# Performance work log

Measured on AMD Instinct MI355X. Metric: run time of the kernel, lower is better.

## Reference

```python
import jax, jax.numpy as jnp
import numpy as np

HIDDEN = 1024
NUM_HEADS = 16
HEAD_SIZE = HIDDEN // NUM_HEADS


def setup_inputs() -> dict:
    key = jax.random.key(0)
    k1, k2, k3 = jax.random.split(key, 3)
    B, S = 2, 2048
    x = jax.random.normal(k1, (B, S, HIDDEN), dtype=jnp.float32)
    # query projection (source reuses it for both q and k)
    Wq = jax.random.normal(k2, (HIDDEN, HIDDEN), dtype=jnp.float32) / np.sqrt(HIDDEN)
    bq = jax.random.normal(k3, (HIDDEN,), dtype=jnp.float32) * 0.01
    return {"x": x, "Wq": Wq, "bq": bq}


def reference(x, Wq, bq):
    B, S, _ = x.shape
    # NOTE: source bug-for-bug: k uses the query projection too
    q = x @ Wq + bq                      # [B,S,D]
    k = x @ Wq + bq                      # [B,S,D]
    q = q.reshape(B, S, NUM_HEADS, HEAD_SIZE)
    k = k.reshape(B, S, NUM_HEADS, HEAD_SIZE)
    # scores: [B,H,S,S]
    e = jnp.einsum("bqhd,bkhd->bhqk", q, k)
    s = jax.nn.softmax(e / jnp.sqrt(jnp.float32(HEAD_SIZE)), axis=-1)
    return s
```

## Files before the change

### kernel.cpp

```cpp
#include <hip/hip_runtime.h>

#define HIDDEN 1024
#define SEQ 2048
#define NB 2
#define PSTRIDE 2052
#define NT 16

typedef _Float16 half8 __attribute__((ext_vector_type(8)));
typedef _Float16 half4 __attribute__((ext_vector_type(4)));
typedef float f32x4 __attribute__((ext_vector_type(4)));

#define GL2LDS(gp, lp) __builtin_amdgcn_global_load_lds( \
    (const __attribute__((address_space(1))) void*)(gp), \
    (__attribute__((address_space(3))) void*)(lp), 16, 0, 0)

__global__ __launch_bounds__(256) void cast_wt(const float* __restrict__ w,
                                               _Float16* __restrict__ wt) {
    __shared__ float tile[32][33];
    int bx = blockIdx.x * 32, by = blockIdx.y * 32;
    int tx = threadIdx.x, ty = threadIdx.y;
    #pragma unroll
    for (int i = 0; i < 32; i += 8)
        tile[ty + i][tx] = w[(by + ty + i) * HIDDEN + bx + tx];
    __syncthreads();
    #pragma unroll
    for (int i = 0; i < 32; i += 8)
        wt[(bx + ty + i) * HIDDEN + by + tx] = (_Float16)tile[tx][ty + i];
}

__global__ __launch_bounds__(512) void proj_gemm(const float* __restrict__ X,
                                                 const _Float16* __restrict__ Bt,
                                                 const float* __restrict__ bias,
                                                 _Float16* __restrict__ Q) {
    __shared__ _Float16 As[128 * 64];
    __shared__ _Float16 Bs[128 * 64];
    const int m0 = blockIdx.x * 128;
    const int n0 = blockIdx.y * 128;
    const int tid = threadIdx.x;
    const int w = tid >> 6, l = tid & 63;
    const int wm = w >> 2, wn = w & 3;
    const int lrow = l & 15, lkslot = l >> 4;

    const int srow = l >> 3, sslot = l & 7;

    f32x4 acc[4][2] = {};

    for (int k0 = 0; k0 < HIDDEN; k0 += 64) {
        __syncthreads();
        #pragma unroll
        for (int j = 0; j < 2; ++j) {
            const int chunk = w * 2 + j;
            const int r = chunk * 8 + srow;
            const int gslot = sslot ^ (r & 7);
            GL2LDS(&Bt[(size_t)(n0 + r) * HIDDEN + k0 + gslot * 8], Bs + chunk * 512);
        }
        #pragma unroll
        for (int it = 0; it < 2; ++it) {
            const int id = it * 512 + tid;
            const int row = id >> 3, slot = id & 7;
            const float* src = &X[(size_t)(m0 + row) * HIDDEN + k0 + slot * 8];
            f32x4 v0 = *(const f32x4*)src;
            f32x4 v1 = *(const f32x4*)(src + 4);
            half8 hv;
            hv[0] = (_Float16)v0[0]; hv[1] = (_Float16)v0[1];
            hv[2] = (_Float16)v0[2]; hv[3] = (_Float16)v0[3];
            hv[4] = (_Float16)v1[0]; hv[5] = (_Float16)v1[1];
            hv[6] = (_Float16)v1[2]; hv[7] = (_Float16)v1[3];
            *(half8*)&As[row * 64 + (slot ^ (row & 7)) * 8] = hv;
        }
        __syncthreads();
        #pragma unroll
        for (int kk = 0; kk < 64; kk += 32) {
            const int csb = kk >> 3;
            half8 af[4], bf[2];
            #pragma unroll
            for (int m = 0; m < 4; ++m) {
                const int R = wm * 64 + m * 16 + lrow;
                const int slot = (csb + lkslot) ^ (R & 7);
                af[m] = *(const half8*)&As[R * 64 + slot * 8];
            }
            #pragma unroll
            for (int n = 0; n < 2; ++n) {
                const int R = wn * 32 + n * 16 + lrow;
                const int slot = (csb + lkslot) ^ (R & 7);
                bf[n] = *(const half8*)&Bs[R * 64 + slot * 8];
            }
            #pragma unroll
            for (int m = 0; m < 4; ++m)
                #pragma unroll
                for (int n = 0; n < 2; ++n)
                    acc[m][n] = __builtin_amdgcn_mfma_f32_16x16x32_f16(af[m], bf[n], acc[m][n], 0, 0, 0);
        }
    }
    const int lr4 = (l >> 4) * 4, lc = l & 15;
    #pragma unroll
    for (int n = 0; n < 2; ++n) {
        int gcol = n0 + wn * 32 + n * 16 + lc;
        float b = bias[gcol];
        #pragma unroll
        for (int m = 0; m < 4; ++m) {
            #pragma unroll
            for (int r = 0; r < 4; ++r) {
                int grow = m0 + wm * 64 + m * 16 + lr4 + r;
                Q[(size_t)grow * HIDDEN + gcol] = (_Float16)(acc[m][n][r] + b);
            }
        }
    }
}

__global__ __launch_bounds__(1024, 4) void scores_softmax(const _Float16* __restrict__ Qh,
                                                          float* __restrict__ out) {
    __shared__ __align__(16) _Float16 p[2][16][PSTRIDE];
    __shared__ float rsum_lds[2][8][16];

    const int raw = blockIdx.x;
    const int xcd = raw & 7, i = raw >> 3;
    const int bh = xcd * 4 + (i >> 3);
    const int qchunk = i & 7;
    const int b = bh >> 4, h = bh & 15;

    const int tid = threadIdx.x;
    const int wv = tid >> 6;
    const int l = tid & 63;
    const int lq = l & 15, lg = l >> 4;
    const int hoff = h * 64;
    const _Float16* qbase = Qh + (size_t)b * SEQ * HIDDEN;
    const size_t outbase = (size_t)(b * 16 + h) * SEQ * SEQ;

    if (wv < 8) {
        const int pw = wv;
        const _Float16* kbase = qbase + (size_t)(pw * 256 + lq) * HIDDEN + hoff + lg * 8;
        for (int t = 0; t <= NT; ++t) {
            if (t < NT) {
                const int buf = t & 1;
                const int q0 = qchunk * 256 + t * 16;
                const _Float16* qp = qbase + (size_t)(q0 + lq) * HIDDEN + hoff + lg * 8;
                const half8 bq0 = *(const half8*)qp;
                const half8 bq1 = *(const half8*)(qp + 32);
                float rsum = 0.f;
                #pragma unroll
                for (int s = 0; s < 16; ++s) {
                    const _Float16* a = kbase + (size_t)s * 16 * HIDDEN;
                    half8 ka = *(const half8*)a;
                    half8 kb = *(const half8*)(a + 32);
                    f32x4 acc = {};
                    acc = __builtin_amdgcn_mfma_f32_16x16x32_f16(ka, bq0, acc, 0, 0, 0);
                    acc = __builtin_amdgcn_mfma_f32_16x16x32_f16(kb, bq1, acc, 0, 0, 0);
                    float e0 = exp2f(fmaf(acc[0], 0.18033688011f, -11.54156033f));
                    float e1 = exp2f(fmaf(acc[1], 0.18033688011f, -11.54156033f));
                    float e2 = exp2f(fmaf(acc[2], 0.18033688011f, -11.54156033f));
                    float e3 = exp2f(fmaf(acc[3], 0.18033688011f, -11.54156033f));
                    rsum += (e0 + e1) + (e2 + e3);
                    half4 hv;
                    hv[0] = (_Float16)e0; hv[1] = (_Float16)e1;
                    hv[2] = (_Float16)e2; hv[3] = (_Float16)e3;
                    *(half4*)&p[buf][lq][pw * 256 + s * 16 + lg * 4] = hv;
                }
                rsum += __shfl_xor(rsum, 16);
                rsum += __shfl_xor(rsum, 32);
                if (l < 16) rsum_lds[buf][pw][l] = rsum;
            }
            asm volatile("s_waitcnt lgkmcnt(0)" ::: "memory");
            __builtin_amdgcn_s_barrier();
        }
    } else {
        const int cw = wv - 8;
        for (int t = 0; t <= NT; ++t) {
            if (t > 0) {
                const int pbuf = (t - 1) & 1;
                #pragma unroll
                for (int rr = 0; rr < 2; ++rr) {
                    const int r = cw * 2 + rr;
                    float rs = 0.f;
                    #pragma unroll
                    for (int w8 = 0; w8 < 8; ++w8) rs += rsum_lds[pbuf][w8][r];
                    const float rinv = 1.0f / rs;
                    float* orow = out + outbase
                                + (size_t)(qchunk * 256 + (t - 1) * 16 + r) * SEQ;
                    #pragma unroll
                    for (int ii = 0; ii < 8; ++ii) {
                        half4 hv = *(const half4*)&p[pbuf][r][ii * 256 + l * 4];
                        f32x4 v;
                        v[0] = (float)hv[0] * rinv; v[1] = (float)hv[1] * rinv;
                        v[2] = (float)hv[2] * rinv; v[3] = (float)hv[3] * rinv;
                        __builtin_nontemporal_store(v, (f32x4*)(orow + ii * 256 + l * 4));
                    }
                }
            }
            asm volatile("s_waitcnt lgkmcnt(0)" ::: "memory");
            __builtin_amdgcn_s_barrier();
        }
    }
}

extern "C" void kernel_launch(void* const* d_in, const int* in_sizes, int n_in,
                              void* d_out, int out_size, void* d_ws, size_t ws_size,
                              hipStream_t stream) {
    const float* x  = (const float*)d_in[0];
    const float* Wq = (const float*)d_in[1];
    const float* bq = (const float*)d_in[2];
    float* out = (float*)d_out;

    _Float16* qh = (_Float16*)d_ws;
    _Float16* wt = qh + (size_t)4 * 1024 * 1024;

    cast_wt<<<dim3(32, 32), dim3(32, 8), 0, stream>>>(Wq, wt);
    proj_gemm<<<dim3(NB * SEQ / 128, HIDDEN / 128), 512, 0, stream>>>(x, wt, bq, qh);
    scores_softmax<<<256, 1024, 0, stream>>>(qh, out);
}
```

Baseline: 131.4 us.

## Halve softmax block size and single-buffer P with two-barrier handoff

The scores/softmax kernel moves from 1024-thread blocks with a double-buffered probability tile to 512-thread blocks (4 producer and 4 consumer waves) with one buffer, doubling the grid to 512 blocks. Each producer wave now covers 512 keys per strip, and the next Q fragment is prefetched between two barriers. The block-to-XCD mapping changes so each XCD gets contiguous head chunks. The goal is to cut LDS use per block and get finer-grained scheduling, but the single buffer removes the overlap between producers and consumers inside a block, so they now serialize.

Result: slower. 229.0 us (+74.2%).

```diff
diff --git a/kernel.cpp b/kernel.cpp
--- a/kernel.cpp
+++ b/kernel.cpp
@@ -4,7 +4,7 @@
 #define SEQ 2048
 #define NB 2
 #define PSTRIDE 2052
-#define NT 16
+#define NSTRIP 8
 
 typedef _Float16 half8 __attribute__((ext_vector_type(8)));
 typedef _Float16 half4 __attribute__((ext_vector_type(4)));
@@ -108,15 +108,15 @@
     }
 }
 
-__global__ __launch_bounds__(1024, 4) void scores_softmax(const _Float16* __restrict__ Qh,
-                                                          float* __restrict__ out) {
-    __shared__ __align__(16) _Float16 p[2][16][PSTRIDE];
-    __shared__ float rsum_lds[2][8][16];
+__global__ __launch_bounds__(512, 4) void scores_softmax(const _Float16* __restrict__ Qh,
+                                                         float* __restrict__ out) {
+    __shared__ __align__(16) _Float16 p[16][PSTRIDE];
+    __shared__ float rsum_lds[4][16];
 
     const int raw = blockIdx.x;
-    const int xcd = raw & 7, i = raw >> 3;
-    const int bh = xcd * 4 + (i >> 3);
-    const int qchunk = i & 7;
+    const int bid = (raw & 7) * 64 + (raw >> 3);
+    const int bh = bid >> 4;
+    const int qc = bid & 15;
     const int b = bh >> 4, h = bh & 15;
 
     const int tid = threadIdx.x;
@@ -127,64 +127,65 @@
     const _Float16* qbase = Qh + (size_t)b * SEQ * HIDDEN;
     const size_t outbase = (size_t)(b * 16 + h) * SEQ * SEQ;
 
-    if (wv < 8) {
+    if (wv < 4) {
         const int pw = wv;
-        const _Float16* kbase = qbase + (size_t)(pw * 256 + lq) * HIDDEN + hoff + lg * 8;
-        for (int t = 0; t <= NT; ++t) {
-            if (t < NT) {
-                const int buf = t & 1;
-                const int q0 = qchunk * 256 + t * 16;
-                const _Float16* qp = qbase + (size_t)(q0 + lq) * HIDDEN + hoff + lg * 8;
-                const half8 bq0 = *(const half8*)qp;
-                const half8 bq1 = *(const half8*)(qp + 32);
-                float rsum = 0.f;
+        const _Float16* kbase = qbase + (size_t)(pw * 512 + lq) * HIDDEN + hoff + lg * 8;
+        const _Float16* qp = qbase + (size_t)(qc * 128 + lq) * HIDDEN + hoff + lg * 8;
+        half8 q0 = *(const half8*)qp;
+        half8 q1 = *(const half8*)(qp + 32);
+        for (int t = 0; t < NSTRIP; ++t) {
+            float rsum = 0.f;
+            #pragma unroll
+            for (int s = 0; s < 32; ++s) {
+                const _Float16* a = kbase + (size_t)s * 16 * HIDDEN;
+                half8 ka = *(const half8*)a;
+                half8 kb = *(const half8*)(a + 32);
+                f32x4 acc = {};
+                acc = __builtin_amdgcn_mfma_f32_16x16x32_f16(ka, q0, acc, 0, 0, 0);
+                acc = __builtin_amdgcn_mfma_f32_16x16x32_f16(kb, q1, acc, 0, 0, 0);
+                float e0 = exp2f(fmaf(acc[0], 0.18033688011f, -11.54156033f));
+                float e1 = exp2f(fmaf(acc[1], 0.18033688011f, -11.54156033f));
+                float e2 = exp2f(fmaf(acc[2], 0.18033688011f, -11.54156033f));
+                float e3 = exp2f(fmaf(acc[3], 0.18033688011f, -11.54156033f));
+                rsum += (e0 + e1) + (e2 + e3);
+                half4 hv;
+                hv[0] = (_Float16)e0; hv[1] = (_Float16)e1;
+                hv[2] = (_Float16)e2; hv[3] = (_Float16)e3;
+                *(half4*)&p[lq][pw * 512 + s * 16 + lg * 4] = hv;
+            }
+            rsum += __shfl_xor(rsum, 16);
+            rsum += __shfl_xor(rsum, 32);
+            if (l < 16) rsum_lds[pw][l] = rsum;
+
+            asm volatile("s_waitcnt lgkmcnt(0)" ::: "memory");
+            __builtin_amdgcn_s_barrier();
+
+            if (t + 1 < NSTRIP) {
+                const _Float16* qn = qbase + (size_t)(qc * 128 + (t + 1) * 16 + lq) * HIDDEN
+                                   + hoff + lg * 8;
+                q0 = *(const half8*)qn;
+                q1 = *(const half8*)(qn + 32);
+            }
+            __builtin_amdgcn_s_barrier();
+        }
+    } else {
+        const int cw = wv - 4;
+        for (int t = 0; t < NSTRIP; ++t) {
+            __builtin_amdgcn_s_barrier();
+            #pragma unroll
+            for (int rr = 0; rr < 4; ++rr) {
+                const int r = cw * 4 + rr;
+                const float rs = rsum_lds[0][r] + rsum_lds[1][r]
+                               + rsum_lds[2][r] + rsum_lds[3][r];
+                const float rinv = 1.0f / rs;
+                float* orow = out + outbase + (size_t)(qc * 128 + t * 16 + r) * SEQ;
                 #pragma unroll
-                for (int s = 0; s < 16; ++s) {
-                    const _Float16* a = kbase + (size_t)s * 16 * HIDDEN;
-                    half8 ka = *(const half8*)a;
-                    half8 kb = *(const half8*)(a + 32);
-                    f32x4 acc = {};
-                    acc = __builtin_amdgcn_mfma_f32_16x16x32_f16(ka, bq0, acc, 0, 0, 0);
-                    acc = __builtin_amdgcn_mfma_f32_16x16x32_f16(kb, bq1, acc, 0, 0, 0);
-                    float e0 = exp2f(fmaf(acc[0], 0.18033688011f, -11.54156033f));
-                    float e1 = exp2f(fmaf(acc[1], 0.18033688011f, -11.54156033f));
-                    float e2 = exp2f(fmaf(acc[2], 0.18033688011f, -11.54156033f));
-                    float e3 = exp2f(fmaf(acc[3], 0.18033688011f, -11.54156033f));
-                    rsum += (e0 + e1) + (e2 + e3);
-                    half4 hv;
-                    hv[0] = (_Float16)e0; hv[1] = (_Float16)e1;
-                    hv[2] = (_Float16)e2; hv[3] = (_Float16)e3;
-                    *(half4*)&p[buf][lq][pw * 256 + s * 16 + lg * 4] = hv;
-                }
-                rsum += __shfl_xor(rsum, 16);
-                rsum += __shfl_xor(rsum, 32);
-                if (l < 16) rsum_lds[buf][pw][l] = rsum;
-            }
-            asm volatile("s_waitcnt lgkmcnt(0)" ::: "memory");
-            __builtin_amdgcn_s_barrier();
-        }
-    } else {
-        const int cw = wv - 8;
-        for (int t = 0; t <= NT; ++t) {
-            if (t > 0) {
-                const int pbuf = (t - 1) & 1;
-                #pragma unroll
-                for (int rr = 0; rr < 2; ++rr) {
-                    const int r = cw * 2 + rr;
-                    float rs = 0.f;
-                    #pragma unroll
-                    for (int w8 = 0; w8 < 8; ++w8) rs += rsum_lds[pbuf][w8][r];
-                    const float rinv = 1.0f / rs;
-                    float* orow = out + outbase
-                                + (size_t)(qchunk * 256 + (t - 1) * 16 + r) * SEQ;
-                    #pragma unroll
-                    for (int ii = 0; ii < 8; ++ii) {
-                        half4 hv = *(const half4*)&p[pbuf][r][ii * 256 + l * 4];
-                        f32x4 v;
-                        v[0] = (float)hv[0] * rinv; v[1] = (float)hv[1] * rinv;
-                        v[2] = (float)hv[2] * rinv; v[3] = (float)hv[3] * rinv;
-                        __builtin_nontemporal_store(v, (f32x4*)(orow + ii * 256 + l * 4));
-                    }
+                for (int ii = 0; ii < 8; ++ii) {
+                    half4 hv = *(const half4*)&p[r][ii * 256 + l * 4];
+                    f32x4 v;
+                    v[0] = (float)hv[0] * rinv; v[1] = (float)hv[1] * rinv;
+                    v[2] = (float)hv[2] * rinv; v[3] = (float)hv[3] * rinv;
+                    __builtin_nontemporal_store(v, (f32x4*)(orow + ii * 256 + l * 4));
                 }
             }
             asm volatile("s_waitcnt lgkmcnt(0)" ::: "memory");
@@ -206,5 +207,5 @@
 
     cast_wt<<<dim3(32, 32), dim3(32, 8), 0, stream>>>(Wq, wt);
     proj_gemm<<<dim3(NB * SEQ / 128, HIDDEN / 128), 512, 0, stream>>>(x, wt, bq, qh);
-    scores_softmax<<<256, 1024, 0, stream>>>(qh, out);
-}
+    scores_softmax<<<512, 512, 0, stream>>>(qh, out);
+}
```
